# Kernel optimization log

Hardware: AMD Instinct MI355X
Metric: run time of the kernel (lower is better)

## Reference

```python
import jax, jax.numpy as jnp
import numpy as np

NL, BS, NQ, D, NH, HD, L, P, DFF, NC = 6, 16, 300, 256, 8, 32, 3, 4, 1024, 80
SHAPES = np.array([[80, 80], [40, 40], [20, 20]], np.int32)  # (H, W) per level: 640x640 input, strides 8/16/32
STARTS = np.array([0, 6400, 8000], np.int32)
LV = 8400  # sum H*W


def setup_inputs():
    keys = iter(jax.random.split(jax.random.key(0), 64))

    def rn(shape, s=0.02):
        return jax.random.normal(next(keys), shape, jnp.float32) * s

    return {
        "tgt": rn((BS, NQ, D), 1.0),
        "ref_points_unact": rn((BS, NQ, 4), 1.0),
        "memory": rn((BS, LV, D), 1.0),
        "spatial_shapes": jnp.asarray(SHAPES),
        "level_start_index": jnp.asarray(STARTS),
        "Wq": rn((NL, D, D)), "bq": rn((NL, D)),
        "Wk": rn((NL, D, D)), "bk": rn((NL, D)),
        "Wv": rn((NL, D, D)), "bv": rn((NL, D)),
        "Wo": rn((NL, D, D)), "bo": rn((NL, D)),
        "ln1_g": jnp.ones((NL, D)), "ln1_b": jnp.zeros((NL, D)),
        "ln2_g": jnp.ones((NL, D)), "ln2_b": jnp.zeros((NL, D)),
        "ln3_g": jnp.ones((NL, D)), "ln3_b": jnp.zeros((NL, D)),
        "Wvp": rn((NL, D, D)), "bvp": rn((NL, D)),
        "Woff": rn((NL, D, NH * L * P * 2)), "boff": rn((NL, NH * L * P * 2), 0.5),
        "Waw": rn((NL, D, NH * L * P)), "baw": rn((NL, NH * L * P)),
        "Wop": rn((NL, D, D)), "bop": rn((NL, D)),
        "Wff1": rn((NL, D, DFF)), "bff1": rn((NL, DFF)),
        "Wff2": rn((NL, DFF, D)), "bff2": rn((NL, D)),
        "Wb1": rn((NL, D, D)), "bb1": rn((NL, D)),
        "Wb2": rn((NL, D, D)), "bb2": rn((NL, D)),
        "Wb3": rn((NL, D, 4)), "bb3": rn((NL, 4)),
        "Ws": rn((NL, D, NC)), "bs_": rn((NL, NC)),
        "Wp1": rn((4, 2 * D)), "bp1": rn((2 * D,)),
        "Wp2": rn((2 * D, D)), "bp2": rn((D,)),
    }


def _ln(x, g, b):
    m = x.mean(-1, keepdims=True)
    v = ((x - m) ** 2).mean(-1, keepdims=True)
    return (x - m) * jax.lax.rsqrt(v + 1e-5) * g + b


def _inv_sigmoid(x, eps=1e-5):
    x = jnp.clip(x, 0.0, 1.0)
    return jnp.log(jnp.clip(x, eps, None)) - jnp.log(jnp.clip(1.0 - x, eps, None))


def _forward(shapes, starts, tgt, ref_points_unact, memory, Wq, bq, Wk, bk, Wv, bv, Wo, bo, ln1_g, ln1_b, ln2_g, ln2_b, ln3_g, ln3_b, Wvp, bvp, Woff, boff, Waw, baw, Wop, bop, Wff1, bff1, Wff2, bff2, Wb1, bb1, Wb2, bb2, Wb3, bb3, Ws, bs_, Wp1, bp1, Wp2, bp2):
    bs, Lq, _ = tgt.shape

    def mha(q, k, v, i):
        qh = (q @ Wq[i] + bq[i]).reshape(bs, Lq, NH, HD)
        kh = (k @ Wk[i] + bk[i]).reshape(bs, Lq, NH, HD)
        vh = (v @ Wv[i] + bv[i]).reshape(bs, Lq, NH, HD)
        att = jax.nn.softmax(jnp.einsum('bqhd,bkhd->bhqk', qh, kh) / np.float32(np.sqrt(HD)), -1)
        return jnp.einsum('bhqk,bkhd->bqhd', att, vh).reshape(bs, Lq, D) @ Wo[i] + bo[i]

    def deform(query, ref, i):
        # multi-scale deformable attention (Deformable-DETR core, bilinear, zero padding)
        val = (memory @ Wvp[i] + bvp[i]).reshape(bs, -1, NH, HD).transpose(0, 2, 1, 3)  # [bs,NH,Lv,HD]
        off = (query @ Woff[i] + boff[i]).reshape(bs, Lq, NH, L, P, 2)
        aw = jax.nn.softmax((query @ Waw[i] + baw[i]).reshape(bs, Lq, NH, L * P), -1).reshape(bs, Lq, NH, L, P)
        r = ref[:, :, None, None, None, :]  # [bs,Lq,1,1,1,4] box (cx,cy,w,h)
        loc = r[..., :2] + off / P * r[..., 2:] * 0.5  # [bs,Lq,NH,L,P,2]
        out = jnp.zeros((bs, NH, Lq, HD), query.dtype)
        for lvl in range(L):
            H, W = int(shapes[lvl, 0]), int(shapes[lvl, 1])
            s = int(starts[lvl])
            vl = val[:, :, s:s + H * W]  # [bs,NH,H*W,HD]
            x = loc[:, :, :, lvl, :, 0].transpose(0, 2, 1, 3) * W - 0.5  # [bs,NH,Lq,P] (align_corners=False)
            y = loc[:, :, :, lvl, :, 1].transpose(0, 2, 1, 3) * H - 0.5
            x0 = jnp.floor(x).astype(jnp.int32)
            y0 = jnp.floor(y).astype(jnp.int32)
            wx, wy = x - x0, y - y0

            def g(xi, yi):
                valid = ((xi >= 0) & (xi < W) & (yi >= 0) & (yi < H)).astype(query.dtype)
                idx = jnp.clip(yi, 0, H - 1) * W + jnp.clip(xi, 0, W - 1)
                gat = jnp.take_along_axis(vl, idx.reshape(bs, NH, Lq * P, 1), axis=2)
                return gat.reshape(bs, NH, Lq, P, HD) * valid[..., None]

            samp = (g(x0, y0) * ((1 - wx) * (1 - wy))[..., None]
                    + g(x0 + 1, y0) * (wx * (1 - wy))[..., None]
                    + g(x0, y0 + 1) * ((1 - wx) * wy)[..., None]
                    + g(x0 + 1, y0 + 1) * (wx * wy)[..., None])
            awl = aw[:, :, :, lvl].transpose(0, 2, 1, 3)  # [bs,NH,Lq,P]
            out = out + (samp * awl[..., None]).sum(3)
        return out.transpose(0, 2, 1, 3).reshape(bs, Lq, D) @ Wop[i] + bop[i]

    ref_d = jax.nn.sigmoid(ref_points_unact)
    out = tgt
    bboxes = logits = None
    for i in range(NL):
        qpos = jax.nn.relu(ref_d @ Wp1 + bp1) @ Wp2 + bp2  # query_pos_head MLP(4 -> 512 -> 256)
        q = out + qpos
        out = _ln(out + mha(q, q, out, i), ln1_g[i], ln1_b[i])
        out = _ln(out + deform(out + qpos, ref_d, i), ln2_g[i], ln2_b[i])
        out = _ln(out + jax.nn.relu(out @ Wff1[i] + bff1[i]) @ Wff2[i] + bff2[i], ln3_g[i], ln3_b[i])
        h = jax.nn.relu(out @ Wb1[i] + bb1[i])
        h = jax.nn.relu(h @ Wb2[i] + bb2[i])
        inter = jax.nn.sigmoid(h @ Wb3[i] + bb3[i] + _inv_sigmoid(ref_d))
        if i == NL - 1:  # eval_idx = -1 -> outputs taken at last layer (inference path)
            bboxes = inter[None]
            logits = (out @ Ws[i] + bs_[i])[None]
        ref_d = inter
    return bboxes, logits


def reference(tgt, ref_points_unact, memory, spatial_shapes, level_start_index, Wq, bq, Wk, bk, Wv, bv, Wo, bo, ln1_g, ln1_b, ln2_g, ln2_b, ln3_g, ln3_b, Wvp, bvp, Woff, boff, Waw, baw, Wop, bop, Wff1, bff1, Wff2, bff2, Wb1, bb1, Wb2, bb2, Wb3, bb3, Ws, bs_, Wp1, bp1, Wp2, bp2):
    shapes = np.asarray(spatial_shapes)
    starts = np.asarray(level_start_index)
    return _forward(shapes, starts, tgt, ref_points_unact, memory, Wq, bq, Wk, bk, Wv, bv, Wo, bo, ln1_g, ln1_b, ln2_g, ln2_b, ln3_g, ln3_b, Wvp, bvp, Woff, boff, Waw, baw, Wop, bop, Wff1, bff1, Wff2, bff2, Wb1, bb1, Wb2, bb2, Wb3, bb3, Ws, bs_, Wp1, bp1, Wp2, bp2)
```

## Files before the change

kernel.cpp:

```cpp
#include <hip/hip_runtime.h>

#define NLAYERS 6
#define BSZ 16
#define NQL 300
#define DM 256
#define NHEAD 8
#define HDIM 32
#define NLVL 3
#define NPT 4
#define DFFN 1024
#define NCLS 80
#define LVTOT 8400
#define NROW (BSZ * NQL)
#define MEMN (BSZ * LVTOT)

typedef __attribute__((ext_vector_type(8))) short bf16x8;
typedef __attribute__((ext_vector_type(8))) ushort us8;
typedef __attribute__((ext_vector_type(4))) float f32x4;

__device__ __forceinline__ float b2f(ushort u) {
    return __uint_as_float(((uint)u) << 16);
}
__device__ __forceinline__ ushort f2b(float f) {
    uint i = __float_as_uint(f);
    uint r = i + 0x7fffu + ((i >> 16) & 1u);
    return (ushort)(r >> 16);
}
__device__ __forceinline__ void split2(float v, ushort& h, ushort& l) {
    ushort hh = f2b(v);
    h = hh;
    l = f2b(v - b2f(hh));
}
__device__ __forceinline__ void gl_lds16(const void* g, void* l) {
    __builtin_amdgcn_global_load_lds(
        (const __attribute__((address_space(1))) unsigned int*)g,
        (__attribute__((address_space(3))) unsigned int*)l, 16, 0, 0);
}

__global__ __launch_bounds__(256) void f2b_kernel(
    const float* __restrict__ src, ushort* __restrict__ dst, int n)
{
    int i = (blockIdx.x * 256 + threadIdx.x) * 4;
    if (i < n) {
        float4 v = *(const float4*)&src[i];
        ushort4 o = {f2b(v.x), f2b(v.y), f2b(v.z), f2b(v.w)};
        *(ushort4*)&dst[i] = o;
    }
}

__global__ __launch_bounds__(256) void split_kernel(
    const float* __restrict__ src, ushort* __restrict__ dh,
    ushort* __restrict__ dl, int n)
{
    int i = (blockIdx.x * 256 + threadIdx.x) * 4;
    if (i < n) {
        float4 v = *(const float4*)&src[i];
        ushort4 h, l;
        split2(v.x, h.x, l.x);
        split2(v.y, h.y, l.y);
        split2(v.z, h.z, l.z);
        split2(v.w, h.w, l.w);
        *(ushort4*)&dh[i] = h;
        *(ushort4*)&dl[i] = l;
    }
}

#define NTE 14
struct TTab {
    const float* s[NTE];
    ushort* d[NTE];
    int K[NTE], N[NTE], dls[NTE], dr0[NTE];
    int tstart[NTE + 1];
};

__global__ __launch_bounds__(256) void transpose_batch_kernel(TTab tab)
{
    __shared__ float tile[32][33];
    const int bx = blockIdx.x;
    int e = 0;
    while (e < NTE - 1 && bx >= tab.tstart[e + 1]) ++e;
    const int local = bx - tab.tstart[e];
    const int K = tab.K[e], N = tab.N[e];
    const int tx_n = (N + 31) >> 5, ty_n = (K + 31) >> 5;
    const int perB = tx_n * ty_n;
    const int z = local / perB;
    const int rem = local - z * perB;
    const int tyi = rem / tx_n, txi = rem - tyi * tx_n;
    const float* src = tab.s[e] + (size_t)z * K * N;
    ushort* dh = tab.d[e] + (size_t)z * tab.dls[e] + (size_t)tab.dr0[e] * K;
    const int n0 = txi * 32, k0 = tyi * 32;
    const int tx = threadIdx.x, ty = threadIdx.y;
    for (int r = 0; r < 32; r += 8) {
        int k = k0 + ty + r, n = n0 + tx;
        if (k < K && n < N) tile[ty + r][tx] = src[(size_t)k * N + n];
    }
    __syncthreads();
    for (int r = 0; r < 32; r += 8) {
        int n = n0 + ty + r, k = k0 + tx;
        if (n < N && k < K) dh[(size_t)n * K + k] = f2b(tile[tx][ty + r]);
    }
}

__global__ __launch_bounds__(256) void concat_both_kernel(
    const float* __restrict__ bq, const float* __restrict__ bk, float* __restrict__ bqk,
    const float* __restrict__ boff, const float* __restrict__ baw, float* __restrict__ bfa)
{
    const int bx = blockIdx.x;
    if (bx < 12) {
        int i = bx * 256 + threadIdx.x;
        if (i < 6 * 512) {
            int l = i / 512, j = i - l * 512;
            bqk[i] = (j < 256) ? bq[l * 256 + j] : bk[l * 256 + j - 256];
        }
    } else {
        int i = (bx - 12) * 256 + threadIdx.x;
        if (i < 6 * 288) {
            int l = i / 288, j = i - l * 288;
            bfa[i] = (j < 192) ? boff[l * 192 + j] : baw[l * 96 + j - 192];
        }
    }
}

template <int ACT>
__global__ __launch_bounds__(256) void gemm_ps(
    const ushort* __restrict__ Ahp, const ushort* __restrict__ Alp,
    const ushort* __restrict__ BTh, const float* __restrict__ bias,
    int M, int N, int K,
    float* __restrict__ Cf, const float* __restrict__ addsrc,
    ushort* __restrict__ Ch, ushort* __restrict__ Cl)
{
    __shared__ __align__(16) ushort Ahs[2][64 * 32];
    __shared__ __align__(16) ushort Als[2][64 * 32];
    __shared__ __align__(16) ushort Bhs[2][64 * 32];

    const int tid  = threadIdx.x;
    const int m0   = blockIdx.x * 64;
    const int n0   = blockIdx.y * 64;
    const int wv   = tid >> 6;
    const int lane = tid & 63;
    const int lm   = lane & 15;
    const int lq   = lane >> 4;
    const int r    = tid >> 2;
    const int c8   = (tid & 3) * 8;

    gl_lds16(&Ahp[(size_t)(m0 + r) * K + c8], &Ahs[0][r * 32 + c8]);
    gl_lds16(&Alp[(size_t)(m0 + r) * K + c8], &Als[0][r * 32 + c8]);
    gl_lds16(&BTh[(size_t)(n0 + r) * K + c8], &Bhs[0][r * 32 + c8]);
    __syncthreads();

    f32x4 acc[4] = {};
    int buf = 0;
    for (int k0 = 32; k0 < K + 32; k0 += 32) {
        const int nxt = buf ^ 1;
        if (k0 < K) {
            gl_lds16(&Ahp[(size_t)(m0 + r) * K + k0 + c8], &Ahs[nxt][r * 32 + c8]);
            gl_lds16(&Alp[(size_t)(m0 + r) * K + k0 + c8], &Als[nxt][r * 32 + c8]);
            gl_lds16(&BTh[(size_t)(n0 + r) * K + k0 + c8], &Bhs[nxt][r * 32 + c8]);
        }
        bf16x8 afh = *(const bf16x8*)&Ahs[buf][(wv * 16 + lm) * 32 + lq * 8];
        bf16x8 afl = *(const bf16x8*)&Als[buf][(wv * 16 + lm) * 32 + lq * 8];
#pragma unroll
        for (int nb = 0; nb < 4; ++nb) {
            bf16x8 bfh = *(const bf16x8*)&Bhs[buf][(nb * 16 + lm) * 32 + lq * 8];
            acc[nb] = __builtin_amdgcn_mfma_f32_16x16x32_bf16(afh, bfh, acc[nb], 0, 0, 0);
            acc[nb] = __builtin_amdgcn_mfma_f32_16x16x32_bf16(afl, bfh, acc[nb], 0, 0, 0);
        }
        __syncthreads();
        buf = nxt;
    }

    const int row = m0 + wv * 16 + lq * 4;
#pragma unroll
    for (int nb = 0; nb < 4; ++nb) {
        int col = n0 + nb * 16 + lm;
        if (col < N) {
            float bv = bias ? bias[col] : 0.f;
#pragma unroll
            for (int rr = 0; rr < 4; ++rr) {
                float v = acc[nb][rr] + bv;
                if (ACT) v = fmaxf(v, 0.f);
                const size_t idx = (size_t)(row + rr) * N + col;
                if (Cf) Cf[idx] = v;
                if (Ch) {
                    float w = addsrc ? (v + addsrc[idx]) : v;
                    ushort h, l;
                    split2(w, h, l);
                    Ch[idx] = h;
                    if (Cl) Cl[idx] = l;
                }
            }
        }
    }
}

__global__ __launch_bounds__(256) void gemm_mix(
    const ushort* __restrict__ Ahp, const ushort* __restrict__ Alp,
    const ushort* __restrict__ BTh, const float* __restrict__ bias,
    int N, int K,
    float* __restrict__ Cf, const float* __restrict__ addsrc,
    ushort* __restrict__ Ch, ushort* __restrict__ Cl,
    int nSmall,
    const ushort* __restrict__ gA, const ushort* __restrict__ gB,
    const float* __restrict__ gbias, ushort* __restrict__ gC,
    int chunkOff)
{
    __shared__ __align__(16) ushort lds[12288];

    const int tid  = threadIdx.x;
    const int wv   = tid >> 6;
    const int lane = tid & 63;
    const int lm   = lane & 15;
    const int lq   = lane >> 4;

    if ((int)blockIdx.x < nSmall) {
        typedef ushort (*lds2)[64 * 32];
        lds2 Ahs = (lds2)lds;
        lds2 Als = (lds2)(lds + 4096);
        lds2 Bhs = (lds2)(lds + 8192);
        const int m0 = (blockIdx.x % 75) * 64;
        const int n0 = (blockIdx.x / 75) * 64;
        const int r  = tid >> 2;
        const int c8 = (tid & 3) * 8;

        gl_lds16(&Ahp[(size_t)(m0 + r) * K + c8], &Ahs[0][r * 32 + c8]);
        gl_lds16(&Alp[(size_t)(m0 + r) * K + c8], &Als[0][r * 32 + c8]);
        gl_lds16(&BTh[(size_t)(n0 + r) * K + c8], &Bhs[0][r * 32 + c8]);
        __syncthreads();

        f32x4 acc[4] = {};
        int buf = 0;
        for (int k0 = 32; k0 < K + 32; k0 += 32) {
            const int nxt = buf ^ 1;
            if (k0 < K) {
                gl_lds16(&Ahp[(size_t)(m0 + r) * K + k0 + c8], &Ahs[nxt][r * 32 + c8]);
                gl_lds16(&Alp[(size_t)(m0 + r) * K + k0 + c8], &Als[nxt][r * 32 + c8]);
                gl_lds16(&BTh[(size_t)(n0 + r) * K + k0 + c8], &Bhs[nxt][r * 32 + c8]);
            }
            bf16x8 afh = *(const bf16x8*)&Ahs[buf][(wv * 16 + lm) * 32 + lq * 8];
            bf16x8 afl = *(const bf16x8*)&Als[buf][(wv * 16 + lm) * 32 + lq * 8];
#pragma unroll
            for (int nb = 0; nb < 4; ++nb) {
                bf16x8 bfh = *(const bf16x8*)&Bhs[buf][(nb * 16 + lm) * 32 + lq * 8];
                acc[nb] = __builtin_amdgcn_mfma_f32_16x16x32_bf16(afh, bfh, acc[nb], 0, 0, 0);
                acc[nb] = __builtin_amdgcn_mfma_f32_16x16x32_bf16(afl, bfh, acc[nb], 0, 0, 0);
            }
            __syncthreads();
            buf = nxt;
        }

        const int row = m0 + wv * 16 + lq * 4;
#pragma unroll
        for (int nb = 0; nb < 4; ++nb) {
            int col = n0 + nb * 16 + lm;
            if (col < N) {
                float bv = bias[col];
#pragma unroll
                for (int rr = 0; rr < 4; ++rr) {
                    float v = acc[nb][rr] + bv;
                    const size_t idx = (size_t)(row + rr) * N + col;
                    if (Cf) Cf[idx] = v;
                    if (Ch) {
                        float w = addsrc ? (v + addsrc[idx]) : v;
                        ushort h, l;
                        split2(w, h, l);
                        Ch[idx] = h;
                        if (Cl) Cl[idx] = l;
                    }
                }
            }
        }
    } else {
        ushort* As = lds;
        ushort* Bs = lds + 4096;
        const int bid = (int)blockIdx.x - nSmall + chunkOff;
        const int n0 = (bid & 1) * 128;
        const int m0 = (bid >> 1) * 128;
        const int wr = wv >> 1, wc = wv & 1;
        const int srow = lane >> 2;
        const int scol = (lane & 3) * 8;

        f32x4 acc[4][4] = {};

        for (int k0 = 0; k0 < 256; k0 += 32) {
            __syncthreads();
#pragma unroll
            for (int s2 = 0; s2 < 2; ++s2) {
                const int seg = wv * 2 + s2;
                const int row = seg * 16 + srow;
                gl_lds16(&gA[(size_t)(m0 + row) * 256 + k0 + scol],
                         &As[seg * 512 + lane * 8]);
                gl_lds16(&gB[(size_t)(n0 + row) * 256 + k0 + scol],
                         &Bs[seg * 512 + lane * 8]);
            }
            __syncthreads();

            bf16x8 af[4], bfr[4];
#pragma unroll
            for (int i = 0; i < 4; ++i)
                af[i] = *(const bf16x8*)&As[(wr * 64 + i * 16 + lm) * 32 + lq * 8];
#pragma unroll
            for (int i = 0; i < 4; ++i)
                bfr[i] = *(const bf16x8*)&Bs[(wc * 64 + i * 16 + lm) * 32 + lq * 8];
#pragma unroll
            for (int mi = 0; mi < 4; ++mi)
#pragma unroll
                for (int ni = 0; ni < 4; ++ni)
                    acc[mi][ni] = __builtin_amdgcn_mfma_f32_16x16x32_bf16(
                        af[mi], bfr[ni], acc[mi][ni], 0, 0, 0);
        }

#pragma unroll
        for (int ni = 0; ni < 4; ++ni) {
            const int col = n0 + wc * 64 + ni * 16 + lm;
            const float bv = gbias[col];
#pragma unroll
            for (int mi = 0; mi < 4; ++mi) {
                const int row = m0 + wr * 64 + mi * 16 + lq * 4;
#pragma unroll
                for (int rr = 0; rr < 4; ++rr)
                    gC[(size_t)(row + rr) * 256 + col] = f2b(acc[mi][ni][rr] + bv);
            }
        }
    }
}

__global__ __launch_bounds__(256) void gemm_qkv(
    const ushort* __restrict__ qhp, const ushort* __restrict__ qlp,
    const ushort* __restrict__ ohp, const ushort* __restrict__ olp,
    const ushort* __restrict__ Bqk, const ushort* __restrict__ Bv,
    const float* __restrict__ biasqk, const float* __restrict__ biasv,
    ushort* __restrict__ Cqk, ushort* __restrict__ Cv)
{
    constexpr int K = 256;
    __shared__ __align__(16) ushort Ahs[2][64 * 32];
    __shared__ __align__(16) ushort Als[2][64 * 32];
    __shared__ __align__(16) ushort Bhs[2][64 * 32];

    const int by = blockIdx.y;
    const ushort *Ahp, *Alp, *BTh;
    const float* bias;
    ushort* Ch;
    int N, n0;
    if (by < 8) { Ahp = qhp; Alp = qlp; BTh = Bqk; bias = biasqk; Ch = Cqk; N = 512; n0 = by * 64; }
    else        { Ahp = ohp; Alp = olp; BTh = Bv;  bias = biasv;  Ch = Cv;  N = 256; n0 = (by - 8) * 64; }

    const int tid  = threadIdx.x;
    const int m0   = blockIdx.x * 64;
    const int wv   = tid >> 6;
    const int lane = tid & 63;
    const int lm   = lane & 15;
    const int lq   = lane >> 4;
    const int r    = tid >> 2;
    const int c8   = (tid & 3) * 8;

    gl_lds16(&Ahp[(size_t)(m0 + r) * K + c8], &Ahs[0][r * 32 + c8]);
    gl_lds16(&Alp[(size_t)(m0 + r) * K + c8], &Als[0][r * 32 + c8]);
    gl_lds16(&BTh[(size_t)(n0 + r) * K + c8], &Bhs[0][r * 32 + c8]);
    __syncthreads();

    f32x4 acc[4] = {};
    int buf = 0;
    for (int k0 = 32; k0 < K + 32; k0 += 32) {
        const int nxt = buf ^ 1;
        if (k0 < K) {
            gl_lds16(&Ahp[(size_t)(m0 + r) * K + k0 + c8], &Ahs[nxt][r * 32 + c8]);
            gl_lds16(&Alp[(size_t)(m0 + r) * K + k0 + c8], &Als[nxt][r * 32 + c8]);
            gl_lds16(&BTh[(size_t)(n0 + r) * K + k0 + c8], &Bhs[nxt][r * 32 + c8]);
        }
        bf16x8 afh = *(const bf16x8*)&Ahs[buf][(wv * 16 + lm) * 32 + lq * 8];
        bf16x8 afl = *(const bf16x8*)&Als[buf][(wv * 16 + lm) * 32 + lq * 8];
#pragma unroll
        for (int nb = 0; nb < 4; ++nb) {
            bf16x8 bfh = *(const bf16x8*)&Bhs[buf][(nb * 16 + lm) * 32 + lq * 8];
            acc[nb] = __builtin_amdgcn_mfma_f32_16x16x32_bf16(afh, bfh, acc[nb], 0, 0, 0);
            acc[nb] = __builtin_amdgcn_mfma_f32_16x16x32_bf16(afl, bfh, acc[nb], 0, 0, 0);
        }
        __syncthreads();
        buf = nxt;
    }

    const int row = m0 + wv * 16 + lq * 4;
#pragma unroll
    for (int nb = 0; nb < 4; ++nb) {
        const int col = n0 + nb * 16 + lm;
        const float bv = bias[col];
#pragma unroll
        for (int rr = 0; rr < 4; ++rr)
            Ch[(size_t)(row + rr) * N + col] = f2b(acc[nb][rr] + bv);
    }
}

__global__ __launch_bounds__(256) void mha_mfma_kernel(
    const ushort* __restrict__ qh, int ldq, const ushort* __restrict__ kh, int ldk,
    const ushort* __restrict__ vh, int ldv,
    ushort* __restrict__ outh, ushort* __restrict__ outl)
{
    __shared__ ushort Kh[304 * 36];
    __shared__ ushort Vth[32 * 328];
    __shared__ ushort Pb[4][16 * 168];

    const int tid = threadIdx.x;
    const int wv = tid >> 6, lane = tid & 63;
    const int bh = blockIdx.x >> 1, half = blockIdx.x & 1;
    const int b = bh >> 3, h = bh & 7;
    const size_t qbase = (size_t)b * NQL * ldq + h * HDIM;
    const size_t kbase = (size_t)b * NQL * ldk + h * HDIM;
    const size_t vbase = (size_t)b * NQL * ldv + h * HDIM;
    const size_t obase = (size_t)b * NQL * DM + h * HDIM;

    for (int idx = tid; idx < 304 * 4; idx += 256) {
        const int row = idx >> 2, d0 = (idx & 3) * 8;
        us8 v = {};
        if (row < NQL) v = *(const us8*)&kh[kbase + (size_t)row * ldk + d0];
        ushort* o = &Kh[row * 36 + d0];
#pragma unroll
        for (int x = 0; x < 8; ++x) o[x] = v[x];
    }
    for (int idx = tid; idx < 328 * 4; idx += 256) {
        const int key = idx >> 2, d0 = (idx & 3) * 8;
        us8 v = {};
        if (key < NQL) v = *(const us8*)&vh[vbase + (size_t)key * ldv + d0];
#pragma unroll
        for (int x = 0; x < 8; ++x) Vth[(d0 + x) * 328 + key] = v[x];
    }
    for (int i = lane; i < 16 * 168; i += 64) Pb[wv][i] = 0;
    __syncthreads();

    const int quad = lane >> 4, c = lane & 15;
    const float scale = 0.17677669529663687f;

    const int qt_beg = (half ? 10 : 0) + wv;
    const int qt_end = (half ? 19 : 10);
    for (int qt = qt_beg; qt < qt_end; qt += 4) {
        const int q = qt * 16 + c;
        bf16x8 qf = *(const bf16x8*)&qh[qbase + (size_t)q * ldq + quad * 8];

        f32x4 sc[19];
#pragma unroll
        for (int kt = 0; kt < 19; ++kt) {
            bf16x8 kf = *(const bf16x8*)&Kh[(kt * 16 + c) * 36 + quad * 8];
            f32x4 a = {};
            a = __builtin_amdgcn_mfma_f32_16x16x32_bf16(qf, kf, a, 0, 0, 0);
            sc[kt] = a;
        }
        float inv4[4];
#pragma unroll
        for (int r = 0; r < 4; ++r) {
            float mx = -1e30f;
#pragma unroll
            for (int kt = 0; kt < 19; ++kt) {
                float s = sc[kt][r] * scale;
                if (kt * 16 + c >= NQL) s = -1e30f;
                sc[kt][r] = s;
                mx = fmaxf(mx, s);
            }
#pragma unroll
            for (int m = 1; m < 16; m <<= 1) mx = fmaxf(mx, __shfl_xor(mx, m, 64));
            float l = 0.f;
#pragma unroll
            for (int kt = 0; kt < 19; ++kt) {
                float p = __expf(sc[kt][r] - mx);
                sc[kt][r] = p;
                l += p;
            }
#pragma unroll
            for (int m = 1; m < 16; m <<= 1) l += __shfl_xor(l, m, 64);
            inv4[r] = 1.f / l;
        }

        f32x4 o0 = {}, o1 = {};
#pragma unroll
        for (int r = 0; r < 4; ++r)
#pragma unroll
            for (int kt = 0; kt < 10; ++kt)
                Pb[wv][(quad * 4 + r) * 168 + kt * 16 + c] = f2b(sc[kt][r] * inv4[r]);
#pragma unroll
        for (int ks = 0; ks < 5; ++ks) {
            bf16x8 pf = *(const bf16x8*)&Pb[wv][c * 168 + ks * 32 + quad * 8];
            bf16x8 v0 = *(const bf16x8*)&Vth[c * 328 + ks * 32 + quad * 8];
            bf16x8 v1 = *(const bf16x8*)&Vth[(16 + c) * 328 + ks * 32 + quad * 8];
            o0 = __builtin_amdgcn_mfma_f32_16x16x32_bf16(pf, v0, o0, 0, 0, 0);
            o1 = __builtin_amdgcn_mfma_f32_16x16x32_bf16(pf, v1, o1, 0, 0, 0);
        }
#pragma unroll
        for (int r = 0; r < 4; ++r) {
#pragma unroll
            for (int kt = 10; kt < 19; ++kt)
                Pb[wv][(quad * 4 + r) * 168 + (kt - 10) * 16 + c] = f2b(sc[kt][r] * inv4[r]);
            Pb[wv][(quad * 4 + r) * 168 + 144 + c] = 0;
        }
#pragma unroll
        for (int ks = 0; ks < 5; ++ks) {
            bf16x8 pf = *(const bf16x8*)&Pb[wv][c * 168 + ks * 32 + quad * 8];
            bf16x8 v0 = *(const bf16x8*)&Vth[c * 328 + 160 + ks * 32 + quad * 8];
            bf16x8 v1 = *(const bf16x8*)&Vth[(16 + c) * 328 + 160 + ks * 32 + quad * 8];
            o0 = __builtin_amdgcn_mfma_f32_16x16x32_bf16(pf, v0, o0, 0, 0, 0);
            o1 = __builtin_amdgcn_mfma_f32_16x16x32_bf16(pf, v1, o1, 0, 0, 0);
        }
#pragma unroll
        for (int r = 0; r < 4; ++r) {
            const int qq = qt * 16 + quad * 4 + r;
            if (qq < NQL) {
                ushort hh, ll;
                split2(o0[r], hh, ll);
                outh[obase + (size_t)qq * DM + c] = hh;
                outl[obase + (size_t)qq * DM + c] = ll;
                split2(o1[r], hh, ll);
                outh[obase + (size_t)qq * DM + 16 + c] = hh;
                outl[obase + (size_t)qq * DM + 16 + c] = ll;
            }
        }
    }
}

__global__ __launch_bounds__(256) void deform_kernel(
    const ushort* __restrict__ val, const float* __restrict__ offaw,
    const float* __restrict__ refd,
    ushort* __restrict__ samph, ushort* __restrict__ sampl)
{
    __shared__ float offs[192];
    __shared__ float aws[96];
    __shared__ float rr[4];
    const int row = blockIdx.x;
    const int b = row / NQL;
    const int t = threadIdx.x;
    if (t < 192) offs[t] = offaw[(size_t)row * 288 + t];
    if (t < 96)  aws[t] = offaw[(size_t)row * 288 + 192 + t];
    if (t < 4)   rr[t] = refd[row * 4 + t];
    __syncthreads();

    const int h = t >> 5, d = t & 31;
    float mx = -1e30f;
#pragma unroll
    for (int j = 0; j < 12; ++j) mx = fmaxf(mx, aws[h * 12 + j]);
    float ev[12]; float se = 0.f;
#pragma unroll
    for (int j = 0; j < 12; ++j) { ev[j] = __expf(aws[h * 12 + j] - mx); se += ev[j]; }
    const float inv = 1.f / se;

    const int HWs[3] = {80, 40, 20};
    const int STs[3] = {0, 6400, 8000};
    float acc = 0.f;
#pragma unroll
    for (int l = 0; l < NLVL; ++l) {
        const int Wd = HWs[l], Hd = HWs[l], st = STs[l];
#pragma unroll
        for (int p = 0; p < NPT; ++p) {
            const float w12 = ev[l * 4 + p] * inv;
            const float ox = offs[((h * 3 + l) * 4 + p) * 2 + 0];
            const float oy = offs[((h * 3 + l) * 4 + p) * 2 + 1];
            const float x = (rr[0] + ox * 0.125f * rr[2]) * Wd - 0.5f;
            const float y = (rr[1] + oy * 0.125f * rr[3]) * Hd - 0.5f;
            const float xf = floorf(x), yf = floorf(y);
            const int x0 = (int)xf, y0 = (int)yf;
            const float wx = x - xf, wy = y - yf;
            const float tw[4] = {(1 - wx) * (1 - wy), wx * (1 - wy),
                                 (1 - wx) * wy,       wx * wy};
            const int xs[4] = {x0, x0 + 1, x0, x0 + 1};
            const int ys[4] = {y0, y0, y0 + 1, y0 + 1};
            float sv = 0.f;
#pragma unroll
            for (int tp = 0; tp < 4; ++tp) {
                const int xi = xs[tp], yi = ys[tp];
                if (xi >= 0 && xi < Wd && yi >= 0 && yi < Hd) {
                    const int idx = st + yi * Wd + xi;
                    sv += tw[tp] * b2f(val[((size_t)b * LVTOT + idx) * DM + h * HDIM + d]);
                }
            }
            acc += w12 * sv;
        }
    }
    ushort hh, ll;
    split2(acc, hh, ll);
    samph[(size_t)row * DM + t] = hh;
    sampl[(size_t)row * DM + t] = ll;
}

__global__ __launch_bounds__(256) void addln_kernel(
    const float* x, const float* __restrict__ dl,
    const float* __restrict__ g, const float* __restrict__ bb,
    float* outf, ushort* __restrict__ outh, ushort* __restrict__ outl,
    const float* __restrict__ qpos, ushort* __restrict__ q2h, ushort* __restrict__ q2l)
{
    const int wv = threadIdx.x >> 6, lane = threadIdx.x & 63;
    const int row = blockIdx.x * 4 + wv;
    const size_t base = (size_t)row * DM + lane * 4;
    const float4 xv = *(const float4*)(x + base);
    const float4 dv = *(const float4*)(dl + base);
    float v[4] = {xv.x + dv.x, xv.y + dv.y, xv.z + dv.z, xv.w + dv.w};

    float s = v[0] + v[1] + v[2] + v[3];
#pragma unroll
    for (int m = 32; m; m >>= 1) s += __shfl_xor(s, m, 64);
    const float mean = s * (1.f / 256.f);
    float sq = 0.f;
#pragma unroll
    for (int j = 0; j < 4; ++j) { float dd = v[j] - mean; sq += dd * dd; }
#pragma unroll
    for (int m = 32; m; m >>= 1) sq += __shfl_xor(sq, m, 64);
    const float rstd = rsqrtf(sq * (1.f / 256.f) + 1e-5f);

    float y[4];
    ushort4 yh, yl;
#pragma unroll
    for (int j = 0; j < 4; ++j) {
        const int col = lane * 4 + j;
        y[j] = (v[j] - mean) * rstd * g[col] + bb[col];
    }
    *(float4*)(outf + base) = make_float4(y[0], y[1], y[2], y[3]);
    split2(y[0], yh.x, yl.x);
    split2(y[1], yh.y, yl.y);
    split2(y[2], yh.z, yl.z);
    split2(y[3], yh.w, yl.w);
    *(ushort4*)(outh + base) = yh;
    *(ushort4*)(outl + base) = yl;
    if (q2h) {
        const float4 qp = *(const float4*)(qpos + base);
        float q2v[4] = {y[0] + qp.x, y[1] + qp.y, y[2] + qp.z, y[3] + qp.w};
        ushort4 qh_, ql_;
        split2(q2v[0], qh_.x, ql_.x);
        split2(q2v[1], qh_.y, ql_.y);
        split2(q2v[2], qh_.z, ql_.z);
        split2(q2v[3], qh_.w, ql_.w);
        *(ushort4*)(q2h + base) = qh_;
        *(ushort4*)(q2l + base) = ql_;
    }
}

__global__ __launch_bounds__(256) void bbox_fused(
    const ushort* __restrict__ h2h, const ushort* __restrict__ h2l,
    const float* __restrict__ Wb3, const float* __restrict__ bb3,
    const float* __restrict__ rpu, float* __restrict__ refd,
    float* __restrict__ dout, int mode, int writeout,
    const float* __restrict__ Wp1, const float* __restrict__ bp1,
    ushort* __restrict__ t1h, ushort* __restrict__ t1l, int computeT1)
{
    __shared__ float hls[64 * 258];
    __shared__ float wb3s[1024];
    __shared__ float wp1s[4 * 512];
    __shared__ float bp1s[512];
    __shared__ float ref4[64 * 4];

    const int tid = threadIdx.x;
    const int r0 = blockIdx.x * 64;

    if (computeT1) {
        for (int i = tid; i < 2048; i += 256) wp1s[i] = Wp1[i];
        if (tid < 256) { bp1s[tid] = bp1[tid]; bp1s[tid + 256] = bp1[tid + 256]; }
    }
    if (mode == 1) {
        for (int i = tid; i < 1024; i += 256) wb3s[i] = Wb3[i];
        for (int j = tid; j < 2048; j += 256) {
            const int row = j >> 5, seg = (j & 31) * 8;
            const size_t g = (size_t)(r0 + row) * 256 + seg;
            us8 hv = *(const us8*)&h2h[g];
            us8 lv = *(const us8*)&h2l[g];
            float* o = &hls[row * 258 + seg];
#pragma unroll
            for (int x = 0; x < 8; ++x) o[x] = b2f(hv[x]) + b2f(lv[x]);
        }
    }
    __syncthreads();

    const int r = tid >> 2, c = tid & 3;
    float v;
    if (mode == 1) {
        float a0 = 0.f, a1 = 0.f, a2 = 0.f, a3 = 0.f;
        const float* hrow = &hls[r * 258];
#pragma unroll 8
        for (int k = 0; k < 256; k += 4) {
            a0 = fmaf(hrow[k + 0], wb3s[(k + 0) * 4 + c], a0);
            a1 = fmaf(hrow[k + 1], wb3s[(k + 1) * 4 + c], a1);
            a2 = fmaf(hrow[k + 2], wb3s[(k + 2) * 4 + c], a2);
            a3 = fmaf(hrow[k + 3], wb3s[(k + 3) * 4 + c], a3);
        }
        const float b3v = (a0 + a1) + (a2 + a3) + bb3[c];
        const float old = refd[(size_t)(r0 + r) * 4 + c];
        const float rc = fminf(fmaxf(old, 0.f), 1.f);
        const float invs = logf(fmaxf(rc, 1e-5f)) - logf(fmaxf(1.f - rc, 1e-5f));
        v = 1.f / (1.f + __expf(-(b3v + invs)));
    } else {
        v = 1.f / (1.f + __expf(-rpu[(size_t)(r0 + r) * 4 + c]));
    }
    refd[(size_t)(r0 + r) * 4 + c] = v;
    if (writeout) dout[(size_t)(r0 + r) * 4 + c] = v;
    ref4[r * 4 + c] = v;
    __syncthreads();

    if (!computeT1) return;
#pragma unroll
    for (int jj = 0; jj < 16; ++jj) {
        const int idx = jj * 2048 + tid * 8;
        const int row = idx >> 9, nb = idx & 511;
        const float a0 = ref4[row * 4 + 0], a1 = ref4[row * 4 + 1];
        const float a2 = ref4[row * 4 + 2], a3 = ref4[row * 4 + 3];
        us8 hv, lv;
#pragma unroll
        for (int x = 0; x < 8; ++x) {
            const int n = nb + x;
            float t = bp1s[n];
            t = fmaf(a0, wp1s[n], t);
            t = fmaf(a1, wp1s[512 + n], t);
            t = fmaf(a2, wp1s[1024 + n], t);
            t = fmaf(a3, wp1s[1536 + n], t);
            t = fmaxf(t, 0.f);
            ushort hh, ll;
            split2(t, hh, ll);
            hv[x] = hh; lv[x] = ll;
        }
        const size_t gg = (size_t)(r0 + row) * 512 + nb;
        *(us8*)&t1h[gg] = hv;
        *(us8*)&t1l[gg] = lv;
    }
}

extern "C" void kernel_launch(void* const* d_in, const int* in_sizes, int n_in,
                              void* d_out, int out_size, void* d_ws, size_t ws_size,
                              hipStream_t stream)
{
    const float* tgt    = (const float*)d_in[0];
    const float* rpu    = (const float*)d_in[1];
    const float* memory = (const float*)d_in[2];
    const float* Wq  = (const float*)d_in[5];  const float* bq  = (const float*)d_in[6];
    const float* Wk  = (const float*)d_in[7];  const float* bk  = (const float*)d_in[8];
    const float* Wv  = (const float*)d_in[9];  const float* bv  = (const float*)d_in[10];
    const float* Wo  = (const float*)d_in[11]; const float* bo  = (const float*)d_in[12];
    const float* ln1g = (const float*)d_in[13]; const float* ln1b = (const float*)d_in[14];
    const float* ln2g = (const float*)d_in[15]; const float* ln2b = (const float*)d_in[16];
    const float* ln3g = (const float*)d_in[17]; const float* ln3b = (const float*)d_in[18];
    const float* Wvp = (const float*)d_in[19]; const float* bvp = (const float*)d_in[20];
    const float* Woff = (const float*)d_in[21]; const float* boff = (const float*)d_in[22];
    const float* Waw = (const float*)d_in[23]; const float* baw = (const float*)d_in[24];
    const float* Wop = (const float*)d_in[25]; const float* bop = (const float*)d_in[26];
    const float* Wff1 = (const float*)d_in[27]; const float* bff1 = (const float*)d_in[28];
    const float* Wff2 = (const float*)d_in[29]; const float* bff2 = (const float*)d_in[30];
    const float* Wb1 = (const float*)d_in[31]; const float* bb1 = (const float*)d_in[32];
    const float* Wb2 = (const float*)d_in[33]; const float* bb2 = (const float*)d_in[34];
    const float* Wb3 = (const float*)d_in[35]; const float* bb3 = (const float*)d_in[36];
    const float* Ws  = (const float*)d_in[37]; const float* bs_ = (const float*)d_in[38];
    const float* Wp1 = (const float*)d_in[39]; const float* bp1 = (const float*)d_in[40];
    const float* Wp2 = (const float*)d_in[41]; const float* bp2 = (const float*)d_in[42];

    size_t off = 0;
    auto alloc = [&](size_t elems, size_t elsz) -> void* {
        void* r = (char*)d_ws + off;
        off += elems * elsz;
        off = (off + 255) & ~(size_t)255;
        return r;
    };
    ushort *wqkh = (ushort*)alloc(6 * 131072, 2);
    ushort *wvh  = (ushort*)alloc(6 * 65536, 2);
    ushort *woh  = (ushort*)alloc(6 * 65536, 2);
    ushort *wvph = (ushort*)alloc(6 * 65536, 2);
    ushort *wfah = (ushort*)alloc(6 * 81920, 2);
    ushort *woph = (ushort*)alloc(6 * 65536, 2);
    ushort *wf1h = (ushort*)alloc(6 * 262144, 2);
    ushort *wf2h = (ushort*)alloc(6 * 262144, 2);
    ushort *wb1h = (ushort*)alloc(6 * 65536, 2);
    ushort *wb2h = (ushort*)alloc(6 * 65536, 2);
    ushort *wsh  = (ushort*)alloc(6 * 20480, 2);
    ushort *wp2h = (ushort*)alloc(131072, 2);
    float  *bqk  = (float*)alloc(6 * 512, 4);
    float  *bfa  = (float*)alloc(6 * 288, 4);

    ushort* mem_bf = (ushort*)alloc((size_t)MEMN * DM, 2);
    ushort* val_bf = (ushort*)alloc((size_t)MEMN * DM, 2);
    float*  out_f  = (float*)alloc(NROW * DM, 4);
    float*  qpos_f = (float*)alloc(NROW * DM, 4);
    float*  tmp_f  = (float*)alloc(NROW * DM, 4);
    float*  refd_f = (float*)alloc(NROW * 4, 4);
    float*  offaw_f = (float*)alloc(NROW * 288, 4);

    ushort* out_h = (ushort*)alloc(NROW * DM, 2);
    ushort* out_l = (ushort*)alloc(NROW * DM, 2);

    const size_t NN = NROW;
    ushort* scratch = (ushort*)alloc(NN * 2056, 2);
    ushort* q_h  = scratch;
    ushort* q_l  = scratch + NN * 256;
    ushort* vh_h = scratch + NN * 512;
    ushort* att_h = scratch;
    ushort* att_l = scratch + NN * 256;
    ushort* q2_h = scratch + NN * 512;
    ushort* q2_l = scratch + NN * 768;
    ushort* samp_h = scratch;
    ushort* samp_l = scratch + NN * 256;
    ushort* ff_h = scratch;
    ushort* ff_l = scratch + NN * 1024;
    ushort* h1_h = scratch;
    ushort* h1_l = scratch + NN * 256;
    ushort* h2_h = scratch + NN * 512;
    ushort* h2_l = scratch + NN * 768;
    ushort* t1_h = scratch + NN * 1024;
    ushort* t1_l = scratch + NN * 1536;
    ushort* qk_h = scratch + NN * 1024;

    if (off > ws_size) return;

    {
        TTab tab;
        const float* ss[NTE] = {Wq, Wk, Wv, Wo, Wvp, Woff, Waw, Wop,
                                Wff1, Wff2, Wb1, Wb2, Ws, Wp2};
        ushort* dd[NTE] = {wqkh, wqkh, wvh, woh, wvph, wfah, wfah, woph,
                           wf1h, wf2h, wb1h, wb2h, wsh, wp2h};
        const int KK[NTE]  = {256, 256, 256, 256, 256, 256, 256, 256,
                              256, 1024, 256, 256, 256, 512};
        const int NNe[NTE] = {256, 256, 256, 256, 256, 192, 96, 256,
                              1024, 256, 256, 256, 80, 256};
        const int BB[NTE]  = {6, 6, 6, 6, 6, 6, 6, 6, 6, 6, 6, 6, 6, 1};
        const int DL[NTE]  = {131072, 131072, 65536, 65536, 65536, 81920, 81920,
                              65536, 262144, 262144, 65536, 65536, 20480, 131072};
        const int DR[NTE]  = {0, 256, 0, 0, 0, 0, 192, 0, 0, 0, 0, 0, 0, 0};
        int total = 0;
        for (int e = 0; e < NTE; ++e) {
            tab.s[e] = ss[e]; tab.d[e] = dd[e];
            tab.K[e] = KK[e]; tab.N[e] = NNe[e];
            tab.dls[e] = DL[e]; tab.dr0[e] = DR[e];
            tab.tstart[e] = total;
            total += ((NNe[e] + 31) / 32) * ((KK[e] + 31) / 32) * BB[e];
        }
        tab.tstart[NTE] = total;
        transpose_batch_kernel<<<total, dim3(32, 8), 0, stream>>>(tab);
    }
    concat_both_kernel<<<19, 256, 0, stream>>>(bq, bk, bqk, boff, baw, bfa);
    f2b_kernel<<<(MEMN * DM) / 1024, 256, 0, stream>>>(memory, mem_bf, MEMN * DM);

    hipMemcpyAsync(out_f, tgt, (size_t)NROW * DM * 4, hipMemcpyDeviceToDevice, stream);
    split_kernel<<<(NROW * DM) / 1024, 256, 0, stream>>>(tgt, out_h, out_l, NROW * DM);
    bbox_fused<<<75, 256, 0, stream>>>(nullptr, nullptr, Wb3, bb3, rpu, refd_f,
                                       nullptr, 0, 0, Wp1, bp1, t1_h, t1_l, 1);

    auto GP = [&](const ushort* Ahp, const ushort* Alp, const ushort* BTh,
                  const float* bias, int N, int K, bool relu,
                  float* Cf, ushort* Ch = nullptr, ushort* Cl = nullptr,
                  const float* addsrc = nullptr) {
        dim3 g(NROW / 64, (N + 63) / 64);
        if (relu) gemm_ps<1><<<g, 256, 0, stream>>>(Ahp, Alp, BTh, bias, NROW, N, K,
                                                    Cf, addsrc, Ch, Cl);
        else      gemm_ps<0><<<g, 256, 0, stream>>>(Ahp, Alp, BTh, bias, NROW, N, K,
                                                    Cf, addsrc, Ch, Cl);
    };

    for (int i = 0; i < NLAYERS; ++i) {
        const ushort* wvp_i = wvph + i * 65536;
        const float*  bvp_i = bvp + i * 256;
        gemm_mix<<<300 + 700, 256, 0, stream>>>(
            t1_h, t1_l, wp2h, bp2, 256, 512, qpos_f, out_f, q_h, q_l,
            300, mem_bf, wvp_i, bvp_i, val_bf, 0);
        gemm_qkv<<<dim3(NROW / 64, 12), 256, 0, stream>>>(
            q_h, q_l, out_h, out_l, wqkh + i * 131072, wvh + i * 65536,
            bqk + i * 512, bv + i * 256, qk_h, vh_h);
        mha_mfma_kernel<<<256, 256, 0, stream>>>(qk_h, 512, qk_h + 256, 512,
                                                 vh_h, 256, att_h, att_l);
        gemm_mix<<<300 + 700, 256, 0, stream>>>(
            att_h, att_l, woh + i * 65536, bo + i * 256, 256, 256, tmp_f,
            nullptr, nullptr, nullptr,
            300, mem_bf, wvp_i, bvp_i, val_bf, 700);
        addln_kernel<<<1200, 256, 0, stream>>>(out_f, tmp_f, ln1g + i * 256, ln1b + i * 256,
                                               out_f, out_h, out_l, qpos_f, q2_h, q2_l);
        gemm_mix<<<375 + 700, 256, 0, stream>>>(
            q2_h, q2_l, wfah + i * 81920, bfa + i * 288, 288, 256, offaw_f,
            nullptr, nullptr, nullptr,
            375, mem_bf, wvp_i, bvp_i, val_bf, 1400);
        deform_kernel<<<4800, 256, 0, stream>>>(val_bf, offaw_f, refd_f, samp_h, samp_l);
        GP(samp_h, samp_l, woph + i * 65536, bop + i * 256, 256, 256, false, tmp_f);
        addln_kernel<<<1200, 256, 0, stream>>>(out_f, tmp_f, ln2g + i * 256, ln2b + i * 256,
                                               out_f, out_h, out_l, nullptr, nullptr, nullptr);
        GP(out_h, out_l, wf1h + i * 262144, bff1 + i * 1024, 1024, 256, true,
           nullptr, ff_h, ff_l);
        GP(ff_h, ff_l, wf2h + i * 262144, bff2 + i * 256, 256, 1024, false, tmp_f);
        addln_kernel<<<1200, 256, 0, stream>>>(out_f, tmp_f, ln3g + i * 256, ln3b + i * 256,
                                               out_f, out_h, out_l, nullptr, nullptr, nullptr);
        GP(out_h, out_l, wb1h + i * 65536, bb1 + i * 256, 256, 256, true,
           nullptr, h1_h, h1_l);
        GP(h1_h, h1_l, wb2h + i * 65536, bb2 + i * 256, 256, 256, true,
           nullptr, h2_h, h2_l);
        const int last = (i == NLAYERS - 1);
        bbox_fused<<<75, 256, 0, stream>>>(h2_h, h2_l, Wb3 + i * 1024, bb3 + i * 4,
                                           nullptr, refd_f, (float*)d_out, 1,
                                           last ? 1 : 0, Wp1, bp1, t1_h, t1_l,
                                           last ? 0 : 1);
        if (last) {
            GP(out_h, out_l, wsh + i * 20480, bs_ + i * 80, 80, 256, false,
               (float*)d_out + NROW * 4);
        }
    }
}
```

Measured before the change: 1.986 ms.

## Add 32-row GEMM tile for N=256 projections and vectorize deformable sampling

Adds a gemm_ps32 kernel that uses 32x64 output tiles with double-buffered LDS loads, doubling the grid size for the N=256 GEMMs (output projection, FFN2, bbox MLP, class head). With only 4800 rows, the 64-row tiles gave few blocks, so the smaller tile is meant to fill more CUs. Each wave now does less MFMA work per loaded tile, which adds overhead. The deformable sampling kernel now handles two query rows per block and has each thread load two adjacent bf16 channels as one 32-bit load, halving the grid and widening the loads and stores.

```diff
diff --git a/kernel.cpp b/kernel.cpp
--- a/kernel.cpp
+++ b/kernel.cpp
@@ -193,6 +193,79 @@
     }
 }
 
+template <int ACT>
+__global__ __launch_bounds__(256) void gemm_ps32(
+    const ushort* __restrict__ Ahp, const ushort* __restrict__ Alp,
+    const ushort* __restrict__ BTh, const float* __restrict__ bias,
+    int M, int N, int K,
+    float* __restrict__ Cf, const float* __restrict__ addsrc,
+    ushort* __restrict__ Ch, ushort* __restrict__ Cl)
+{
+    __shared__ __align__(16) ushort Ahs[2][32 * 32];
+    __shared__ __align__(16) ushort Als[2][32 * 32];
+    __shared__ __align__(16) ushort Bhs[2][64 * 32];
+
+    const int tid  = threadIdx.x;
+    const int m0   = blockIdx.x * 32;
+    const int n0   = blockIdx.y * 64;
+    const int wv   = tid >> 6;
+    const int lane = tid & 63;
+    const int lm   = lane & 15;
+    const int lq   = lane >> 4;
+    const int ra   = (tid & 127) >> 2;
+    const int rb   = tid >> 2;
+    const int c8   = (tid & 3) * 8;
+
+    if (tid < 128) gl_lds16(&Ahp[(size_t)(m0 + ra) * K + c8], &Ahs[0][ra * 32 + c8]);
+    else           gl_lds16(&Alp[(size_t)(m0 + ra) * K + c8], &Als[0][ra * 32 + c8]);
+    gl_lds16(&BTh[(size_t)(n0 + rb) * K + c8], &Bhs[0][rb * 32 + c8]);
+    __syncthreads();
+
+    f32x4 acc[2] = {};
+    int buf = 0;
+    for (int k0 = 32; k0 < K + 32; k0 += 32) {
+        const int nxt = buf ^ 1;
+        if (k0 < K) {
+            if (tid < 128) gl_lds16(&Ahp[(size_t)(m0 + ra) * K + k0 + c8], &Ahs[nxt][ra * 32 + c8]);
+            else           gl_lds16(&Alp[(size_t)(m0 + ra) * K + k0 + c8], &Als[nxt][ra * 32 + c8]);
+            gl_lds16(&BTh[(size_t)(n0 + rb) * K + k0 + c8], &Bhs[nxt][rb * 32 + c8]);
+        }
+        bf16x8 bfh = *(const bf16x8*)&Bhs[buf][(wv * 16 + lm) * 32 + lq * 8];
+#pragma unroll
+        for (int mb = 0; mb < 2; ++mb) {
+            bf16x8 afh = *(const bf16x8*)&Ahs[buf][(mb * 16 + lm) * 32 + lq * 8];
+            bf16x8 afl = *(const bf16x8*)&Als[buf][(mb * 16 + lm) * 32 + lq * 8];
+            acc[mb] = __builtin_amdgcn_mfma_f32_16x16x32_bf16(afh, bfh, acc[mb], 0, 0, 0);
+            acc[mb] = __builtin_amdgcn_mfma_f32_16x16x32_bf16(afl, bfh, acc[mb], 0, 0, 0);
+        }
+        __syncthreads();
+        buf = nxt;
+    }
+
+    const int col = n0 + wv * 16 + lm;
+    if (col < N) {
+        const float bv = bias ? bias[col] : 0.f;
+#pragma unroll
+        for (int mb = 0; mb < 2; ++mb) {
+            const int row = m0 + mb * 16 + lq * 4;
+#pragma unroll
+            for (int rr = 0; rr < 4; ++rr) {
+                float v = acc[mb][rr] + bv;
+                if (ACT) v = fmaxf(v, 0.f);
+                const size_t idx = (size_t)(row + rr) * N + col;
+                if (Cf) Cf[idx] = v;
+                if (Ch) {
+                    float w = addsrc ? (v + addsrc[idx]) : v;
+                    ushort h, l;
+                    split2(w, h, l);
+                    Ch[idx] = h;
+                    if (Cl) Cl[idx] = l;
+                }
+            }
+        }
+    }
+}
+
 __global__ __launch_bounds__(256) void gemm_mix(
     const ushort* __restrict__ Ahp, const ushort* __restrict__ Alp,
     const ushort* __restrict__ BTh, const float* __restrict__ bias,
@@ -518,39 +591,51 @@
     const float* __restrict__ refd,
     ushort* __restrict__ samph, ushort* __restrict__ sampl)
 {
-    __shared__ float offs[192];
-    __shared__ float aws[96];
-    __shared__ float rr[4];
-    const int row = blockIdx.x;
+    __shared__ float offs[2][192];
+    __shared__ float aws[2][96];
+    __shared__ float rr4[2][4];
+    const int row0 = blockIdx.x * 2;
+    const int t = threadIdx.x;
+    for (int i = t; i < 2 * 288; i += 256) {
+        const int rh = i / 288, j = i - rh * 288;
+        const float v = offaw[(size_t)(row0 + rh) * 288 + j];
+        if (j < 192) offs[rh][j] = v;
+        else         aws[rh][j - 192] = v;
+    }
+    if (t < 8) rr4[t >> 2][t & 3] = refd[(size_t)(row0 + (t >> 2)) * 4 + (t & 3)];
+    __syncthreads();
+
+    const int half = t >> 7;
+    const int row = row0 + half;
     const int b = row / NQL;
-    const int t = threadIdx.x;
-    if (t < 192) offs[t] = offaw[(size_t)row * 288 + t];
-    if (t < 96)  aws[t] = offaw[(size_t)row * 288 + 192 + t];
-    if (t < 4)   rr[t] = refd[row * 4 + t];
-    __syncthreads();
-
-    const int h = t >> 5, d = t & 31;
+    const int t7 = t & 127;
+    const int h = t7 >> 4;
+    const int d2 = (t7 & 15) * 2;
+
     float mx = -1e30f;
 #pragma unroll
-    for (int j = 0; j < 12; ++j) mx = fmaxf(mx, aws[h * 12 + j]);
+    for (int j = 0; j < 12; ++j) mx = fmaxf(mx, aws[half][h * 12 + j]);
     float ev[12]; float se = 0.f;
 #pragma unroll
-    for (int j = 0; j < 12; ++j) { ev[j] = __expf(aws[h * 12 + j] - mx); se += ev[j]; }
+    for (int j = 0; j < 12; ++j) { ev[j] = __expf(aws[half][h * 12 + j] - mx); se += ev[j]; }
     const float inv = 1.f / se;
+
+    const float r0 = rr4[half][0], r1 = rr4[half][1];
+    const float r2 = rr4[half][2], r3 = rr4[half][3];
 
     const int HWs[3] = {80, 40, 20};
     const int STs[3] = {0, 6400, 8000};
-    float acc = 0.f;
+    float acc0 = 0.f, acc1 = 0.f;
 #pragma unroll
     for (int l = 0; l < NLVL; ++l) {
         const int Wd = HWs[l], Hd = HWs[l], st = STs[l];
 #pragma unroll
         for (int p = 0; p < NPT; ++p) {
             const float w12 = ev[l * 4 + p] * inv;
-            const float ox = offs[((h * 3 + l) * 4 + p) * 2 + 0];
-            const float oy = offs[((h * 3 + l) * 4 + p) * 2 + 1];
-            const float x = (rr[0] + ox * 0.125f * rr[2]) * Wd - 0.5f;
-            const float y = (rr[1] + oy * 0.125f * rr[3]) * Hd - 0.5f;
+            const float ox = offs[half][((h * 3 + l) * 4 + p) * 2 + 0];
+            const float oy = offs[half][((h * 3 + l) * 4 + p) * 2 + 1];
+            const float x = (r0 + ox * 0.125f * r2) * Wd - 0.5f;
+            const float y = (r1 + oy * 0.125f * r3) * Hd - 0.5f;
             const float xf = floorf(x), yf = floorf(y);
             const int x0 = (int)xf, y0 = (int)yf;
             const float wx = x - xf, wy = y - yf;
@@ -558,22 +643,27 @@
                                  (1 - wx) * wy,       wx * wy};
             const int xs[4] = {x0, x0 + 1, x0, x0 + 1};
             const int ys[4] = {y0, y0, y0 + 1, y0 + 1};
-            float sv = 0.f;
+            float sv0 = 0.f, sv1 = 0.f;
 #pragma unroll
             for (int tp = 0; tp < 4; ++tp) {
                 const int xi = xs[tp], yi = ys[tp];
                 if (xi >= 0 && xi < Wd && yi >= 0 && yi < Hd) {
                     const int idx = st + yi * Wd + xi;
-                    sv += tw[tp] * b2f(val[((size_t)b * LVTOT + idx) * DM + h * HDIM + d]);
+                    const uint u = *(const uint*)&val[((size_t)b * LVTOT + idx) * DM + h * HDIM + d2];
+                    sv0 = fmaf(tw[tp], b2f((ushort)u), sv0);
+                    sv1 = fmaf(tw[tp], b2f((ushort)(u >> 16)), sv1);
                 }
             }
-            acc += w12 * sv;
-        }
-    }
-    ushort hh, ll;
-    split2(acc, hh, ll);
-    samph[(size_t)row * DM + t] = hh;
-    sampl[(size_t)row * DM + t] = ll;
+            acc0 = fmaf(w12, sv0, acc0);
+            acc1 = fmaf(w12, sv1, acc1);
+        }
+    }
+    ushort h0, l0, h1, l1;
+    split2(acc0, h0, l0);
+    split2(acc1, h1, l1);
+    const size_t o = (size_t)row * DM + h * HDIM + d2;
+    *(ushort2*)&samph[o] = make_ushort2(h0, h1);
+    *(ushort2*)&sampl[o] = make_ushort2(l0, l1);
 }
 
 __global__ __launch_bounds__(256) void addln_kernel(
@@ -840,6 +930,16 @@
         else      gemm_ps<0><<<g, 256, 0, stream>>>(Ahp, Alp, BTh, bias, NROW, N, K,
                                                     Cf, addsrc, Ch, Cl);
     };
+    auto GP32 = [&](const ushort* Ahp, const ushort* Alp, const ushort* BTh,
+                    const float* bias, int N, int K, bool relu,
+                    float* Cf, ushort* Ch = nullptr, ushort* Cl = nullptr,
+                    const float* addsrc = nullptr) {
+        dim3 g(NROW / 32, (N + 63) / 64);
+        if (relu) gemm_ps32<1><<<g, 256, 0, stream>>>(Ahp, Alp, BTh, bias, NROW, N, K,
+                                                      Cf, addsrc, Ch, Cl);
+        else      gemm_ps32<0><<<g, 256, 0, stream>>>(Ahp, Alp, BTh, bias, NROW, N, K,
+                                                      Cf, addsrc, Ch, Cl);
+    };
 
     for (int i = 0; i < NLAYERS; ++i) {
         const ushort* wvp_i = wvph + i * 65536;
@@ -862,27 +962,27 @@
             q2_h, q2_l, wfah + i * 81920, bfa + i * 288, 288, 256, offaw_f,
             nullptr, nullptr, nullptr,
             375, mem_bf, wvp_i, bvp_i, val_bf, 1400);
-        deform_kernel<<<4800, 256, 0, stream>>>(val_bf, offaw_f, refd_f, samp_h, samp_l);
-        GP(samp_h, samp_l, woph + i * 65536, bop + i * 256, 256, 256, false, tmp_f);
+        deform_kernel<<<2400, 256, 0, stream>>>(val_bf, offaw_f, refd_f, samp_h, samp_l);
+        GP32(samp_h, samp_l, woph + i * 65536, bop + i * 256, 256, 256, false, tmp_f);
         addln_kernel<<<1200, 256, 0, stream>>>(out_f, tmp_f, ln2g + i * 256, ln2b + i * 256,
                                                out_f, out_h, out_l, nullptr, nullptr, nullptr);
         GP(out_h, out_l, wf1h + i * 262144, bff1 + i * 1024, 1024, 256, true,
            nullptr, ff_h, ff_l);
-        GP(ff_h, ff_l, wf2h + i * 262144, bff2 + i * 256, 256, 1024, false, tmp_f);
+        GP32(ff_h, ff_l, wf2h + i * 262144, bff2 + i * 256, 256, 1024, false, tmp_f);
         addln_kernel<<<1200, 256, 0, stream>>>(out_f, tmp_f, ln3g + i * 256, ln3b + i * 256,
                                                out_f, out_h, out_l, nullptr, nullptr, nullptr);
-        GP(out_h, out_l, wb1h + i * 65536, bb1 + i * 256, 256, 256, true,
-           nullptr, h1_h, h1_l);
-        GP(h1_h, h1_l, wb2h + i * 65536, bb2 + i * 256, 256, 256, true,
-           nullptr, h2_h, h2_l);
+        GP32(out_h, out_l, wb1h + i * 65536, bb1 + i * 256, 256, 256, true,
+             nullptr, h1_h, h1_l);
+        GP32(h1_h, h1_l, wb2h + i * 65536, bb2 + i * 256, 256, 256, true,
+             nullptr, h2_h, h2_l);
         const int last = (i == NLAYERS - 1);
         bbox_fused<<<75, 256, 0, stream>>>(h2_h, h2_l, Wb3 + i * 1024, bb3 + i * 4,
                                            nullptr, refd_f, (float*)d_out, 1,
                                            last ? 1 : 0, Wp1, bp1, t1_h, t1_l,
                                            last ? 0 : 1);
         if (last) {
-            GP(out_h, out_l, wsh + i * 20480, bs_ + i * 80, 80, 256, false,
-               (float*)d_out + NROW * 4);
-        }
-    }
-}
+            GP32(out_h, out_l, wsh + i * 20480, bs_ + i * 80, 80, 256, false,
+                 (float*)d_out + NROW * 4);
+        }
+    }
+}
```

Result: faster. 1.855 ms (-6.6%).
